# Kernel tuning notes

Measured on AMD Instinct MI355X. Metric: run time of the kernel, lower is better.

## Reference

```python
import jax, jax.numpy as jnp
import numpy as np

B, S, D = 1, 2048, 2048
H, KVH, HD = 32, 8, 64
FFN = 8192
N_EXPERTS, TOP_K = 32, 4
EPS = 1e-5
NEG = -1e9


def setup_inputs() -> dict:
    key = jax.random.key(0)
    ks = jax.random.split(key, 24)
    s = 0.02
    inp = {}
    inp['hidden_states'] = jax.random.normal(ks[0], (B, S, D), jnp.float32)
    # RoPE tables: cos/sin of shape [B, S, HD]
    inv_freq = 1.0 / (10000.0 ** (np.arange(0, HD, 2, dtype=np.float32) / HD))
    t = np.arange(S, dtype=np.float32)
    freqs = np.outer(t, inv_freq)                      # [S, HD/2]
    emb = np.concatenate([freqs, freqs], axis=-1)      # [S, HD]
    inp['cos'] = jnp.asarray(np.cos(emb))[None].repeat(B, axis=0)
    inp['sin'] = jnp.asarray(np.sin(emb))[None].repeat(B, axis=0)
    # additive causal mask [B, 1, S, S]
    causal = jnp.where(jnp.tril(jnp.ones((S, S), bool)), 0.0, NEG).astype(jnp.float32)
    inp['attention_mask'] = jnp.broadcast_to(causal[None, None], (B, 1, S, S))
    # attention params
    inp['wq'] = jax.random.normal(ks[1], (H * HD, D), jnp.float32) * s
    inp['bq'] = jnp.zeros((H * HD,), jnp.float32)
    inp['wk'] = jax.random.normal(ks[2], (KVH * HD, D), jnp.float32) * s
    inp['bk'] = jnp.zeros((KVH * HD,), jnp.float32)
    inp['wv'] = jax.random.normal(ks[3], (KVH * HD, D), jnp.float32) * s
    inp['bv'] = jnp.zeros((KVH * HD,), jnp.float32)
    inp['wo'] = jax.random.normal(ks[4], (D, H * HD), jnp.float32) * s
    inp['bo'] = jnp.zeros((D,), jnp.float32)
    # norms
    inp['ln1_w'] = jnp.ones((D,), jnp.float32)
    inp['ln2_w'] = jnp.ones((D,), jnp.float32)
    # MoE gate + shared expert MLP
    inp['gate_w'] = jax.random.normal(ks[5], (N_EXPERTS, D), jnp.float32) * s
    inp['gate_b'] = jnp.zeros((N_EXPERTS,), jnp.float32)
    inp['w1'] = jax.random.normal(ks[6], (FFN, D), jnp.float32) * s
    inp['b1'] = jnp.zeros((FFN,), jnp.float32)
    inp['w2'] = jax.random.normal(ks[7], (D, FFN), jnp.float32) * s
    inp['b2'] = jnp.zeros((D,), jnp.float32)
    inp['w3'] = jax.random.normal(ks[8], (FFN, D), jnp.float32) * s
    inp['b3'] = jnp.zeros((FFN,), jnp.float32)
    return inp


def _rms_norm(x, w, eps=EPS):
    x32 = x.astype(jnp.float32)
    var = jnp.mean(x32 * x32, axis=-1, keepdims=True)
    return (w * (x32 * jax.lax.rsqrt(var + eps))).astype(x.dtype)


def _rotate_half(x):
    x1, x2 = jnp.split(x, 2, axis=-1)
    return jnp.concatenate([-x2, x1], axis=-1)


def _decoder_layer(hidden_states, cos, sin, attention_mask,
                   wq, bq, wk, bk, wv, bv, wo, bo, ln1_w, ln2_w,
                   gate_w, gate_b, w1, b1, w2, b2, w3, b3):
    residual = hidden_states
    x = _rms_norm(hidden_states, ln1_w)

    # projections -> [B, heads, S, HD]
    q = (x @ wq.T + bq).reshape(B, S, H, HD).transpose(0, 2, 1, 3)
    k = (x @ wk.T + bk).reshape(B, S, KVH, HD).transpose(0, 2, 1, 3)
    v = (x @ wv.T + bv).reshape(B, S, KVH, HD).transpose(0, 2, 1, 3)

    # RoPE (cos/sin unsqueezed on head dim)
    c, s_ = cos[:, None], sin[:, None]
    q = q * c + _rotate_half(q) * s_
    k = k * c + _rotate_half(k) * s_

    # GQA: repeat kv heads
    n_rep = H // KVH
    k = jnp.repeat(k, n_rep, axis=1)
    v = jnp.repeat(v, n_rep, axis=1)

    scaling = HD ** -0.5
    scores = jnp.einsum('bhqd,bhkd->bhqk', q, k) * scaling + attention_mask
    probs = jax.nn.softmax(scores.astype(jnp.float32), axis=-1).astype(q.dtype)
    attn = jnp.einsum('bhqk,bhkd->bhqd', probs, v)
    attn = attn.transpose(0, 2, 1, 3).reshape(B, S, H * HD)
    attn = attn @ wo.T + bo

    hidden_states = residual + attn
    residual = hidden_states
    x = _rms_norm(hidden_states, ln2_w)

    # MoE block (as written in source: router computed, but ALL tokens go
    # through one shared expert MLP; routing weights unused in output)
    flat = x.reshape(-1, D)
    router_logits = flat @ gate_w.T + gate_b                     # [B*S, E]
    rw = jax.nn.softmax(router_logits.astype(jnp.float32), axis=-1)
    rw_top, sel = jax.lax.top_k(rw, TOP_K)                       # computed, unused
    del rw_top, sel

    h1 = flat @ w1.T + b1
    h3 = flat @ w3.T + b3
    mlp = (jax.nn.silu(h1) * h3) @ w2.T + b2
    hidden_states = residual + mlp.reshape(B, S, D)
    return hidden_states


def reference(hidden_states, cos, sin, attention_mask,
              wq, bq, wk, bk, wv, bv, wo, bo, ln1_w, ln2_w,
              gate_w, gate_b, w1, b1, w2, b2, w3, b3):
    return _decoder_layer(hidden_states, cos, sin, attention_mask,
                          wq, bq, wk, bk, wv, bv, wo, bo, ln1_w, ln2_w,
                          gate_w, gate_b, w1, b1, w2, b2, w3, b3)
```

## Files before the change

### kernel.cpp

```cpp
#include <hip/hip_runtime.h>

#define S_LEN 2048
#define DMODEL 2048
#define NH 32
#define NKV 8
#define HD 64
#define FFN_DIM 8192

typedef __attribute__((ext_vector_type(4))) float f32x4;
typedef __attribute__((ext_vector_type(16))) float f32x16;
typedef __attribute__((ext_vector_type(8))) short bf16x8;

#define MFMA(a, b, c) __builtin_amdgcn_mfma_f32_16x16x32_bf16(a, b, c, 0, 0, 0)
#define MFMA32(a, b, c) __builtin_amdgcn_mfma_f32_32x32x16_bf16(a, b, c, 0, 0, 0)

__device__ __forceinline__ ushort f2bf(float f) {
  unsigned u = __float_as_uint(f);
  unsigned r = (u + 0x7fffu + ((u >> 16) & 1u)) >> 16;
  return (ushort)r;
}
__device__ __forceinline__ float bf2f(ushort s) {
  return __uint_as_float(((unsigned)s) << 16);
}
__device__ __forceinline__ unsigned cvtpk(float a, float b) {
  unsigned r;
  asm("v_cvt_pk_bf16_f32 %0, %1, %2" : "=v"(r) : "v"(a), "v"(b));
  return r;
}

__device__ __forceinline__ void gload16(const void* g, void* l) {
  __builtin_amdgcn_global_load_lds(
      (const __attribute__((address_space(1))) void*)g,
      (__attribute__((address_space(3))) void*)l, 16, 0, 0);
}

__global__ __launch_bounds__(256) void cvt_k(const float* __restrict__ in,
                                             ushort* __restrict__ out) {
  int i = blockIdx.x * 256 + threadIdx.x;
  f32x4 a = ((const f32x4*)in)[i * 2];
  f32x4 b = ((const f32x4*)in)[i * 2 + 1];
  bf16x8 r;
#pragma unroll
  for (int j = 0; j < 4; j++) r[j] = (short)f2bf(a[j]);
#pragma unroll
  for (int j = 0; j < 4; j++) r[4 + j] = (short)f2bf(b[j]);
  ((bf16x8*)out)[i] = r;
}

__global__ __launch_bounds__(256) void cvt_qkv_k(const float* __restrict__ wq,
                                                 const float* __restrict__ wk,
                                                 const float* __restrict__ wv,
                                                 ushort* __restrict__ dst) {
  int row = blockIdx.x;
  const float* src;
  if (row < 2048) src = wq + (size_t)row * DMODEL;
  else if (row < 2560) src = wk + (size_t)(row - 2048) * DMODEL;
  else src = wv + (size_t)(row - 2560) * DMODEL;
  int i = threadIdx.x * 8;
  f32x4 a = *(const f32x4*)(src + i);
  f32x4 b = *(const f32x4*)(src + i + 4);
  bf16x8 r;
#pragma unroll
  for (int j = 0; j < 4; j++) r[j] = (short)f2bf(a[j]);
#pragma unroll
  for (int j = 0; j < 4; j++) r[4 + j] = (short)f2bf(b[j]);
  *(bf16x8*)(dst + (size_t)row * DMODEL + i) = r;
}

__global__ __launch_bounds__(256) void bias3_k(const float* __restrict__ a,
                                               const float* __restrict__ b,
                                               const float* __restrict__ c,
                                               float* __restrict__ out) {
  int i = blockIdx.x * 256 + threadIdx.x;
  float v;
  if (i < 2048) v = a[i];
  else if (i < 2560) v = b[i - 2048];
  else v = c[i - 2560];
  out[i] = v;
}

__global__ __launch_bounds__(256) void rmsnorm_k(const float* __restrict__ in,
                                                 const float* __restrict__ w,
                                                 ushort* __restrict__ out) {
  const int row = blockIdx.x;
  const int tid = threadIdx.x;
  const float* x = in + (size_t)row * DMODEL;
  f32x4 v0 = *(const f32x4*)(x + tid * 8);
  f32x4 v1 = *(const f32x4*)(x + tid * 8 + 4);
  float ss = v0[0] * v0[0] + v0[1] * v0[1] + v0[2] * v0[2] + v0[3] * v0[3] +
             v1[0] * v1[0] + v1[1] * v1[1] + v1[2] * v1[2] + v1[3] * v1[3];
#pragma unroll
  for (int off = 32; off; off >>= 1) ss += __shfl_xor(ss, off, 64);
  __shared__ float red[4];
  if ((tid & 63) == 0) red[tid >> 6] = ss;
  __syncthreads();
  float tot = red[0] + red[1] + red[2] + red[3];
  float inv = rsqrtf(tot * (1.f / DMODEL) + 1e-5f);
#pragma unroll
  for (int i = 0; i < 8; i++) {
    int c = tid * 8 + i;
    float val = (i < 4) ? v0[i] : v1[i - 4];
    out[(size_t)row * DMODEL + c] = f2bf(w[c] * val * inv);
  }
}

__global__ __launch_bounds__(256) void rope_k(ushort* __restrict__ qkv,
                                              const float* __restrict__ cs,
                                              const float* __restrict__ sn) {
  int idx = blockIdx.x * 256 + threadIdx.x;
  int d = idx & 31;
  int t = idx >> 5;
  int head = t % (NH + NKV);
  int s = t / (NH + NKV);
  int col = (head < NH) ? head * HD : DMODEL + (head - NH) * HD;
  ushort* p = qkv + (size_t)s * 3072 + col;
  float lo = bf2f(p[d]), hi = bf2f(p[d + 32]);
  float c = cs[s * HD + d], si = sn[s * HD + d];
  p[d] = f2bf(lo * c - hi * si);
  p[d + 32] = f2bf(hi * c + lo * si);
}

enum { EPI_BF16 = 0, EPI_RESID = 1, EPI_SILU = 2, EPI_MUL = 3, EPI_PART = 4 };

__device__ __forceinline__ void quad(const bf16x8* Arr, const bf16x8* BR,
                                     f32x4 (*accr)[4], int qn) {
#pragma unroll
  for (int i = 0; i < 4; i++)
#pragma unroll
    for (int j = 0; j < 2; j++)
#pragma unroll
      for (int ks = 0; ks < 2; ks++)
        accr[i][qn * 2 + j] =
            MFMA(Arr[2 * i + ks], BR[2 * j + ks], accr[i][qn * 2 + j]);
}

template <int EPI>
__global__ __launch_bounds__(512, 2) void gemm256(
    const ushort* __restrict__ A, int lda, const ushort* __restrict__ B,
    int ldb, const float* __restrict__ bias, const float* __restrict__ resid,
    ushort* __restrict__ outb, float* __restrict__ outf, int ldc, int K,
    int kspan, long long opart) {
  __shared__ __align__(16) ushort lds[65536];
  const int tid = threadIdx.x;
  const int l = tid & 63, w = tid >> 6;
  const int g = l >> 4, r16 = l & 15;
  const int wm = w >> 2, wn = w & 3;

  int nwg = gridDim.x * gridDim.y;
  int bid = blockIdx.y * gridDim.x + blockIdx.x;
  bid = (bid & 7) * (nwg >> 3) + (bid >> 3);
  const int m0 = (bid % gridDim.x) * 256;
  const int n0 = (bid / gridDim.x) * 256;
  const int z = blockIdx.z;

  const ushort* Ag = A + (size_t)z * kspan + (size_t)m0 * lda;
  const ushort* Bg = B + (size_t)z * kspan + (size_t)n0 * ldb;
  ushort* outbz = outb;
  if (EPI == EPI_PART) outbz = outb + (size_t)z * opart;

  const int NT = K >> 6;

  const int stgRow = w * 8 + (l >> 3);
  const int stgCol = ((l & 7) ^ (l >> 3)) * 8;

  const int xa = (r16 & 7) << 4;
  const int c0 = ((g * 16) ^ xa) >> 1;
  const int c1 = c0 ^ 32;
  const int slotA = wm ? 3 : 1;
  const int slotB = (wn >> 1) ? 2 : 0;
  const ushort* pA0 = lds + slotA * 8192 + r16 * 64 + c0;
  const ushort* pA1 = lds + slotA * 8192 + r16 * 64 + c1;
  const ushort* pB0 = lds + slotB * 8192 + ((wn & 1) * 64 + r16) * 64 + c0;
  const ushort* pB1 = lds + slotB * 8192 + ((wn & 1) * 64 + r16) * 64 + c1;

  f32x4 acc[8][4];
#pragma unroll
  for (int i = 0; i < 8; i++)
#pragma unroll
    for (int j = 0; j < 4; j++) acc[i][j] = (f32x4){0, 0, 0, 0};

  auto stageA = [&](int slot, int tile, int hf) {
    ushort* dst = lds + ((tile & 1) * 32768 + slot * 8192 + w * 512);
    const ushort* src =
        Ag + (size_t)(hf * 128 + stgRow) * lda + tile * 64 + stgCol;
    gload16(src, dst);
    gload16(src + (size_t)64 * lda, dst + 4096);
  };
  auto stageB = [&](int slot, int tile, int hf) {
    ushort* dst = lds + ((tile & 1) * 32768 + slot * 8192 + w * 512);
    const ushort* src =
        Bg + (size_t)(hf * 128 + stgRow) * ldb + tile * 64 + stgCol;
    gload16(src, dst);
    gload16(src + (size_t)64 * ldb, dst + 4096);
  };

  stageB(0, 0, 0);
  stageA(1, 0, 0);
  stageB(2, 0, 1);
  stageA(3, 0, 1);
  stageB(0, 1, 0);
  stageA(1, 1, 0);
  asm volatile("s_waitcnt vmcnt(4)" ::: "memory");
  __builtin_amdgcn_s_barrier();

  bf16x8 Ar[8], Br0[4], Br1[4];

  for (int t = 0; t < NT; ++t) {
    const int bo = (t & 1) * 32768;
#pragma unroll
    for (int i = 0; i < 4; i++) {
      Ar[2 * i] = *(const bf16x8*)(pA0 + bo + i * 1024);
      Ar[2 * i + 1] = *(const bf16x8*)(pA1 + bo + i * 1024);
    }
#pragma unroll
    for (int j = 0; j < 2; j++) {
      Br0[2 * j] = *(const bf16x8*)(pB0 + bo + j * 1024);
      Br0[2 * j + 1] = *(const bf16x8*)(pB1 + bo + j * 1024);
    }
    if (t + 1 < NT) stageB(2, t + 1, 1);
    __builtin_amdgcn_s_barrier();
    __builtin_amdgcn_s_setprio(1);
    quad(Ar, Br0, &acc[0], 0);
    __builtin_amdgcn_s_setprio(0);
    __builtin_amdgcn_s_barrier();
#pragma unroll
    for (int j = 0; j < 2; j++) {
      Br1[2 * j] = *(const bf16x8*)(pB0 + bo + (j + 2) * 1024);
      Br1[2 * j + 1] = *(const bf16x8*)(pB1 + bo + (j + 2) * 1024);
    }
    if (t + 1 < NT) stageA(3, t + 1, 1);
    __builtin_amdgcn_s_barrier();
    __builtin_amdgcn_s_setprio(1);
    quad(Ar, Br1, &acc[0], 1);
    __builtin_amdgcn_s_setprio(0);
    __builtin_amdgcn_s_barrier();
#pragma unroll
    for (int i = 0; i < 4; i++) {
      Ar[2 * i] = *(const bf16x8*)(pA0 + bo + (i + 4) * 1024);
      Ar[2 * i + 1] = *(const bf16x8*)(pA1 + bo + (i + 4) * 1024);
    }
    if (t + 2 < NT) stageB(0, t + 2, 0);
    __builtin_amdgcn_s_barrier();
    __builtin_amdgcn_s_setprio(1);
    quad(Ar, Br1, &acc[4], 1);
    __builtin_amdgcn_s_setprio(0);
    __builtin_amdgcn_s_barrier();
    if (t + 2 < NT) stageA(1, t + 2, 0);
    __builtin_amdgcn_s_barrier();
    __builtin_amdgcn_s_setprio(1);
    quad(Ar, Br0, &acc[4], 0);
    __builtin_amdgcn_s_setprio(0);
    if (t + 2 < NT) {
      asm volatile("s_waitcnt vmcnt(4)" ::: "memory");
    } else {
      asm volatile("s_waitcnt vmcnt(0)" ::: "memory");
    }
    __builtin_amdgcn_s_barrier();
  }

#pragma unroll
  for (int mf = 0; mf < 8; mf++) {
#pragma unroll
    for (int nf = 0; nf < 4; nf++) {
      const int n = n0 + wn * 64 + nf * 16 + r16;
      float bia = (EPI == EPI_PART) ? 0.f : bias[n];
#pragma unroll
      for (int reg = 0; reg < 4; reg++) {
        const int m = m0 + wm * 128 + mf * 16 + g * 4 + reg;
        float v = acc[mf][nf][reg] + bia;
        if constexpr (EPI == EPI_BF16) {
          outbz[(size_t)m * ldc + n] = f2bf(v);
        } else if constexpr (EPI == EPI_RESID) {
          outf[(size_t)m * ldc + n] = v + resid[(size_t)m * ldc + n];
        } else if constexpr (EPI == EPI_SILU) {
          float sv = v / (1.f + __expf(-v));
          outbz[(size_t)m * ldc + n] = f2bf(sv);
        } else if constexpr (EPI == EPI_MUL) {
          float hv = bf2f(outbz[(size_t)m * ldc + n]);
          outbz[(size_t)m * ldc + n] = f2bf(v * hv);
        } else {
          outbz[(size_t)m * ldc + n] = f2bf(v);
        }
      }
    }
  }
}

template <int MODE>
__global__ __launch_bounds__(256) void reduce2_k(
    const ushort* __restrict__ part, long long pstride, int nz,
    const float* __restrict__ bias, int ncol, const float* __restrict__ resid,
    float* __restrict__ outf, ushort* __restrict__ outb) {
  long long i = (long long)(blockIdx.x * 256 + threadIdx.x) * 8;
  int col = (int)(i % ncol);
  float s[8];
#pragma unroll
  for (int j = 0; j < 8; j++) s[j] = bias[col + j];
  for (int zz = 0; zz < nz; zz++) {
    bf16x8 v = *(const bf16x8*)(part + zz * pstride + i);
#pragma unroll
    for (int j = 0; j < 8; j++) s[j] += bf2f((ushort)v[j]);
  }
  if constexpr (MODE == 1) {
#pragma unroll
    for (int j = 0; j < 8; j++) outf[i + j] = s[j] + resid[i + j];
  } else {
    bf16x8 r;
#pragma unroll
    for (int j = 0; j < 8; j++) r[j] = (short)f2bf(s[j]);
    *(bf16x8*)(outb + i) = r;
  }
}

__global__ __launch_bounds__(256, 3) void flash2_k(const ushort* __restrict__ qkv,
                                                   ushort* __restrict__ att) {
  const int bid = blockIdx.x;
  const int head = (bid >> 4) & 31;
  const int rmap = bid & 15;
  const int qb = (bid & 256) ? (15 - rmap) : rmap;
  const int kvh = head >> 2;
  const int tid = threadIdx.x;
  const int w = tid >> 6, l = tid & 63;
  const int h = l >> 5, q31 = l & 31;
  const int qw = qb * 128 + w * 32;
  const int qrow = qw + q31;

  __shared__ __align__(16) ushort lds[2][8192];

  bf16x8 qreg[4];
  {
    const ushort* qp = qkv + (size_t)qrow * 3072 + head * HD;
#pragma unroll
    for (int s = 0; s < 4; s++)
      qreg[s] = *(const bf16x8*)(qp + s * 16 + h * 8);
  }

  f32x16 oacc[2];
#pragma unroll
  for (int i = 0; i < 16; i++) { oacc[0][i] = 0.f; oacc[1][i] = 0.f; }
  float mreg = -1e30f, lsum = 0.f;

  const int nt = 2 * qb + 2;

  const int skv = tid >> 2;
  const int sch = (tid & 3) * 2;
  const int vkv = tid & 63;
  const int vd0 = (tid >> 6) * 16;

  const ushort* kg_base = qkv + DMODEL + kvh * HD;

  bf16x8 krA, krB, vrA, vrB;
  auto loadTile = [&](int jb) {
    const ushort* kg = kg_base + (size_t)jb * 64 * 3072;
    krA = *(const bf16x8*)(kg + (size_t)skv * 3072 + sch * 8);
    krB = *(const bf16x8*)(kg + (size_t)skv * 3072 + sch * 8 + 8);
    const ushort* vg = kg + 512;
    vrA = *(const bf16x8*)(vg + (size_t)vkv * 3072 + vd0);
    vrB = *(const bf16x8*)(vg + (size_t)vkv * 3072 + vd0 + 8);
  };
  auto writeTile = [&](int b) {
    ushort* kb = lds[b];
    *(bf16x8*)(kb + skv * 64 + ((sch ^ (skv & 7)) * 8)) = krA;
    *(bf16x8*)(kb + skv * 64 + (((sch + 1) ^ (skv & 7)) * 8)) = krB;
    ushort* vb = lds[b] + 4096;
#pragma unroll
    for (int i = 0; i < 8; i++) {
      int d = vd0 + i;
      vb[d * 64 + (((vkv >> 3) ^ (d & 7)) * 8) + (vkv & 7)] = (ushort)vrA[i];
    }
#pragma unroll
    for (int i = 0; i < 8; i++) {
      int d = vd0 + 8 + i;
      vb[d * 64 + (((vkv >> 3) ^ (d & 7)) * 8) + (vkv & 7)] = (ushort)vrB[i];
    }
  };

  loadTile(0);
  for (int jb = 0; jb < nt; ++jb) {
    const int b = jb & 1;
    writeTile(b);
    __syncthreads();
    if (jb + 1 < nt) loadTile(jb + 1);

    if (jb * 64 <= qw + 31) {
      const ushort* Kb = lds[b];
      const ushort* Vb = lds[b] + 4096;

      f32x16 sacc[2];
#pragma unroll
      for (int i = 0; i < 16; i++) { sacc[0][i] = 0.f; sacc[1][i] = 0.f; }
#pragma unroll
      for (int c = 0; c < 2; c++) {
        const int kvr = c * 32 + q31;
        const ushort* kp = Kb + kvr * 64;
        const int kx = kvr & 7;
#pragma unroll
        for (int s = 0; s < 4; s++) {
          bf16x8 kf = *(const bf16x8*)(kp + ((2 * s + h) ^ kx) * 8);
          sacc[c] = MFMA32(kf, qreg[s], sacc[c]);
        }
      }

      const bool diag = (jb * 64 + 63 > qw);
      if (diag) {
#pragma unroll
        for (int c = 0; c < 2; c++)
#pragma unroll
          for (int rg = 0; rg < 16; rg++) {
            int kvg = jb * 64 + c * 32 + (rg & 3) + 8 * (rg >> 2) + 4 * h;
            if (kvg > qrow) sacc[c][rg] = -1e30f;
          }
      }
      float tmax = sacc[0][0];
#pragma unroll
      for (int rg = 1; rg < 16; rg++) tmax = fmaxf(tmax, sacc[0][rg]);
#pragma unroll
      for (int rg = 0; rg < 16; rg++) tmax = fmaxf(tmax, sacc[1][rg]);
      tmax = fmaxf(tmax, __shfl_xor(tmax, 32));
      const float mn = fmaxf(mreg, tmax);
      const float resc = __expf((mreg - mn) * 0.125f);
      mreg = mn;
      float rsum = 0.f;
#pragma unroll
      for (int c = 0; c < 2; c++)
#pragma unroll
        for (int rg = 0; rg < 16; rg++) {
          float pv = __expf((sacc[c][rg] - mn) * 0.125f);
          sacc[c][rg] = pv;
          rsum += pv;
        }
      rsum += __shfl_xor(rsum, 32);
      lsum = lsum * resc + rsum;
      oacc[0] *= resc;
      oacc[1] *= resc;

      unsigned pw_[2][4][2];
#pragma unroll
      for (int c = 0; c < 2; c++)
#pragma unroll
        for (int rr = 0; rr < 4; rr++) {
          pw_[c][rr][0] = cvtpk(sacc[c][4 * rr + 0], sacc[c][4 * rr + 1]);
          pw_[c][rr][1] = cvtpk(sacc[c][4 * rr + 2], sacc[c][4 * rr + 3]);
        }

#pragma unroll
      for (int s = 0; s < 4; s++) {
        const int c = s >> 1, base = (s & 1) * 2;
        unsigned k0 = h ? pw_[c][base + 1][0] : pw_[c][base][0];
        unsigned k1 = h ? pw_[c][base + 1][1] : pw_[c][base][1];
        unsigned s0 = h ? pw_[c][base][0] : pw_[c][base + 1][0];
        unsigned s1 = h ? pw_[c][base][1] : pw_[c][base + 1][1];
        unsigned t0 = __shfl_xor(s0, 32);
        unsigned t1 = __shfl_xor(s1, 32);
        union { unsigned u[4]; bf16x8 v; } pf;
        pf.u[0] = h ? t0 : k0;
        pf.u[1] = h ? t1 : k1;
        pf.u[2] = h ? k0 : t0;
        pf.u[3] = h ? k1 : t1;
#pragma unroll
        for (int dt = 0; dt < 2; dt++) {
          const int d = dt * 32 + q31;
          bf16x8 vf =
              *(const bf16x8*)(Vb + d * 64 + ((2 * s + h) ^ (d & 7)) * 8);
          oacc[dt] = MFMA32(vf, pf.v, oacc[dt]);
        }
      }
    }
  }

  const float inv = 1.f / lsum;
  ushort* op = att + (size_t)qrow * DMODEL + head * HD;
#pragma unroll
  for (int dt = 0; dt < 2; dt++)
#pragma unroll
    for (int rr = 0; rr < 4; rr++) {
      const int d0 = dt * 32 + 8 * rr + 4 * h;
      unsigned lo = cvtpk(oacc[dt][4 * rr + 0] * inv, oacc[dt][4 * rr + 1] * inv);
      unsigned hi = cvtpk(oacc[dt][4 * rr + 2] * inv, oacc[dt][4 * rr + 3] * inv);
      uint2 v2;
      v2.x = lo;
      v2.y = hi;
      *(uint2*)(op + d0) = v2;
    }
}

extern "C" void kernel_launch(void* const* d_in, const int* in_sizes, int n_in,
                              void* d_out, int out_size, void* d_ws,
                              size_t ws_size, hipStream_t stream) {
  (void)in_sizes; (void)n_in; (void)out_size; (void)ws_size;
  const float* hidden = (const float*)d_in[0];
  const float* cosb = (const float*)d_in[1];
  const float* sinb = (const float*)d_in[2];
  const float* wq = (const float*)d_in[4];
  const float* bq = (const float*)d_in[5];
  const float* wk = (const float*)d_in[6];
  const float* bk = (const float*)d_in[7];
  const float* wv = (const float*)d_in[8];
  const float* bv = (const float*)d_in[9];
  const float* wo = (const float*)d_in[10];
  const float* bo = (const float*)d_in[11];
  const float* ln1 = (const float*)d_in[12];
  const float* ln2 = (const float*)d_in[13];
  const float* w1 = (const float*)d_in[16];
  const float* b1 = (const float*)d_in[17];
  const float* w2 = (const float*)d_in[18];
  const float* b2 = (const float*)d_in[19];
  const float* w3 = (const float*)d_in[20];
  const float* b3 = (const float*)d_in[21];
  float* out = (float*)d_out;

  char* ws = (char*)d_ws;
  ushort* x1 = (ushort*)ws;   ws += (size_t)S_LEN * DMODEL * 2;
  ushort* qkv = (ushort*)ws;  ws += (size_t)S_LEN * 3072 * 2;
  ushort* att = (ushort*)ws;  ws += (size_t)S_LEN * DMODEL * 2;
  ushort* x2 = (ushort*)ws;   ws += (size_t)S_LEN * DMODEL * 2;
  ushort* hbuf = (ushort*)ws; ws += (size_t)S_LEN * FFN_DIM * 2;
  ushort* wbuf = (ushort*)ws; ws += (size_t)FFN_DIM * DMODEL * 2;
  float* bqkv = (float*)ws;   ws += 3072 * 4;

  ushort* partQ = att;
  ushort* partO = x2;
  ushort* partW = x1;

  rmsnorm_k<<<S_LEN, 256, 0, stream>>>(hidden, ln1, x1);

  cvt_qkv_k<<<3072, 256, 0, stream>>>(wq, wk, wv, wbuf);
  bias3_k<<<12, 256, 0, stream>>>(bq, bk, bv, bqkv);

  gemm256<EPI_PART><<<dim3(8, 12, 2), 512, 0, stream>>>(
      x1, DMODEL, wbuf, DMODEL, nullptr, nullptr, partQ, nullptr, 3072, 1024,
      1024, (long long)S_LEN * 3072);
  reduce2_k<0><<<(S_LEN * 3072) / 2048, 256, 0, stream>>>(
      partQ, (long long)S_LEN * 3072, 2, bqkv, 3072, nullptr, nullptr, qkv);

  rope_k<<<(S_LEN * (NH + NKV) * 32) / 256, 256, 0, stream>>>(qkv, cosb, sinb);

  flash2_k<<<512, 256, 0, stream>>>(qkv, att);

  cvt_k<<<(2048 * 2048) / 2048, 256, 0, stream>>>(wo, wbuf);
  gemm256<EPI_PART><<<dim3(8, 8, 4), 512, 0, stream>>>(
      att, DMODEL, wbuf, DMODEL, nullptr, nullptr, partO, nullptr, DMODEL, 512,
      512, (long long)S_LEN * DMODEL);
  reduce2_k<1><<<(S_LEN * DMODEL) / 2048, 256, 0, stream>>>(
      partO, (long long)S_LEN * DMODEL, 4, bo, DMODEL, hidden, out, nullptr);

  rmsnorm_k<<<S_LEN, 256, 0, stream>>>(out, ln2, x2);

  cvt_k<<<(FFN_DIM * 2048) / 2048, 256, 0, stream>>>(w1, wbuf);
  gemm256<EPI_SILU><<<dim3(8, 32), 512, 0, stream>>>(
      x2, DMODEL, wbuf, DMODEL, b1, nullptr, hbuf, nullptr, FFN_DIM, DMODEL, 0,
      0);

  cvt_k<<<(FFN_DIM * 2048) / 2048, 256, 0, stream>>>(w3, wbuf);
  gemm256<EPI_MUL><<<dim3(8, 32), 512, 0, stream>>>(
      x2, DMODEL, wbuf, DMODEL, b3, nullptr, hbuf, nullptr, FFN_DIM, DMODEL, 0,
      0);

  cvt_k<<<(DMODEL * FFN_DIM) / 2048, 256, 0, stream>>>(w2, wbuf);
  gemm256<EPI_PART><<<dim3(8, 8, 4), 512, 0, stream>>>(
      hbuf, FFN_DIM, wbuf, FFN_DIM, nullptr, nullptr, partW, nullptr, DMODEL,
      DMODEL, DMODEL, (long long)S_LEN * DMODEL);
  reduce2_k<1><<<(S_LEN * DMODEL) / 2048, 256, 0, stream>>>(
      partW, (long long)S_LEN * DMODEL, 4, b2, DMODEL, out, out, nullptr);
}
```

Baseline: 425.3 us.

## Prefetch full tiles two iterations ahead and fence LDS reads per MFMA cluster

Changes the GEMM software pipeline so that both halves of the A and B tiles are prefetched two K-iterations ahead, instead of splitting the second halves one iteration ahead. The vmcnt wait goes from 4 to 8 outstanding loads to match. It also wraps each MFMA cluster in a helper that waits for LDS reads and adds a scheduling barrier, so register loads finish before the math starts. The aim is to hide global-load latency behind more work, at the cost of more loads in flight and more rigid instruction scheduling.

```diff
diff --git a/kernel.cpp b/kernel.cpp
--- a/kernel.cpp
+++ b/kernel.cpp
@@ -134,6 +134,17 @@
             MFMA(Arr[2 * i + ks], BR[2 * j + ks], accr[i][qn * 2 + j]);
 }
 
+__device__ __forceinline__ void cluster_begin() {
+  __builtin_amdgcn_s_barrier();
+  asm volatile("s_waitcnt lgkmcnt(0)" ::: "memory");
+  __builtin_amdgcn_sched_barrier(0);
+  __builtin_amdgcn_s_setprio(1);
+}
+__device__ __forceinline__ void cluster_end() {
+  __builtin_amdgcn_s_setprio(0);
+  __builtin_amdgcn_s_barrier();
+}
+
 template <int EPI>
 __global__ __launch_bounds__(512, 2) void gemm256(
     const ushort* __restrict__ A, int lda, const ushort* __restrict__ B,
@@ -195,12 +206,14 @@
   };
 
   stageB(0, 0, 0);
+  stageB(2, 0, 1);
   stageA(1, 0, 0);
-  stageB(2, 0, 1);
   stageA(3, 0, 1);
   stageB(0, 1, 0);
+  stageB(2, 1, 1);
   stageA(1, 1, 0);
-  asm volatile("s_waitcnt vmcnt(4)" ::: "memory");
+  stageA(3, 1, 1);
+  asm volatile("s_waitcnt vmcnt(8)" ::: "memory");
   __builtin_amdgcn_s_barrier();
 
   bf16x8 Ar[8], Br0[4], Br1[4];
@@ -217,41 +230,39 @@
       Br0[2 * j] = *(const bf16x8*)(pB0 + bo + j * 1024);
       Br0[2 * j + 1] = *(const bf16x8*)(pB1 + bo + j * 1024);
     }
-    if (t + 1 < NT) stageB(2, t + 1, 1);
-    __builtin_amdgcn_s_barrier();
-    __builtin_amdgcn_s_setprio(1);
+    cluster_begin();
     quad(Ar, Br0, &acc[0], 0);
-    __builtin_amdgcn_s_setprio(0);
-    __builtin_amdgcn_s_barrier();
+    cluster_end();
 #pragma unroll
     for (int j = 0; j < 2; j++) {
       Br1[2 * j] = *(const bf16x8*)(pB0 + bo + (j + 2) * 1024);
       Br1[2 * j + 1] = *(const bf16x8*)(pB1 + bo + (j + 2) * 1024);
     }
-    if (t + 1 < NT) stageA(3, t + 1, 1);
-    __builtin_amdgcn_s_barrier();
-    __builtin_amdgcn_s_setprio(1);
+    cluster_begin();
     quad(Ar, Br1, &acc[0], 1);
-    __builtin_amdgcn_s_setprio(0);
-    __builtin_amdgcn_s_barrier();
+    cluster_end();
 #pragma unroll
     for (int i = 0; i < 4; i++) {
       Ar[2 * i] = *(const bf16x8*)(pA0 + bo + (i + 4) * 1024);
       Ar[2 * i + 1] = *(const bf16x8*)(pA1 + bo + (i + 4) * 1024);
     }
-    if (t + 2 < NT) stageB(0, t + 2, 0);
-    __builtin_amdgcn_s_barrier();
-    __builtin_amdgcn_s_setprio(1);
+    if (t + 2 < NT) {
+      stageB(0, t + 2, 0);
+      stageB(2, t + 2, 1);
+    }
+    cluster_begin();
     quad(Ar, Br1, &acc[4], 1);
-    __builtin_amdgcn_s_setprio(0);
-    __builtin_amdgcn_s_barrier();
-    if (t + 2 < NT) stageA(1, t + 2, 0);
+    cluster_end();
+    if (t + 2 < NT) {
+      stageA(1, t + 2, 0);
+      stageA(3, t + 2, 1);
+    }
     __builtin_amdgcn_s_barrier();
     __builtin_amdgcn_s_setprio(1);
     quad(Ar, Br0, &acc[4], 0);
     __builtin_amdgcn_s_setprio(0);
     if (t + 2 < NT) {
-      asm volatile("s_waitcnt vmcnt(4)" ::: "memory");
+      asm volatile("s_waitcnt vmcnt(8)" ::: "memory");
     } else {
       asm volatile("s_waitcnt vmcnt(0)" ::: "memory");
     }
```

Result: no change. 430.0 us (+1.1%).

## Restructure GEMM main loop into software-pipelined two-tile phases with register prefetch

Applied to the files above, without the earlier changes.

Rewrites the 256x256 bf16 GEMM main loop to process two K-tiles per iteration, using separate register sets for even and odd A fragments and prefetching LDS fragments for the next phase while the current MFMA quad runs. Global staging now prefetches both halves of a tile ahead, with full vmcnt drains at tile boundaries, and scheduling barriers plus lgkmcnt waits pin the instruction order. The aim is to hide LDS read latency and global-load latency behind MFMA work. The cost is higher register pressure and a fixed lgkmcnt count that must match the number of LDS reads actually issued. The loop also assumes an even tile count.

```diff
diff --git a/kernel.cpp b/kernel.cpp
--- a/kernel.cpp
+++ b/kernel.cpp
@@ -122,17 +122,31 @@
 
 enum { EPI_BF16 = 0, EPI_RESID = 1, EPI_SILU = 2, EPI_MUL = 3, EPI_PART = 4 };
 
-__device__ __forceinline__ void quad(const bf16x8* Arr, const bf16x8* BR,
-                                     f32x4 (*accr)[4], int qn) {
-#pragma unroll
-  for (int i = 0; i < 4; i++)
-#pragma unroll
-    for (int j = 0; j < 2; j++)
-#pragma unroll
-      for (int ks = 0; ks < 2; ks++)
-        accr[i][qn * 2 + j] =
-            MFMA(Arr[2 * i + ks], BR[2 * j + ks], accr[i][qn * 2 + j]);
-}
+#define QUAD(AS, BS, MROW, NCOL)                                     \
+  _Pragma("unroll") for (int mf_ = 0; mf_ < 4; mf_++)                \
+  _Pragma("unroll") for (int nf_ = 0; nf_ < 2; nf_++)                \
+  _Pragma("unroll") for (int kk_ = 0; kk_ < 2; kk_++)                \
+      acc[(MROW) + mf_][(NCOL) + nf_] =                              \
+          MFMA(AS[2 * mf_ + kk_], BS[2 * nf_ + kk_],                 \
+               acc[(MROW) + mf_][(NCOL) + nf_]);
+
+#define PHASE_SYNC                                   \
+  __builtin_amdgcn_sched_barrier(0);                 \
+  __builtin_amdgcn_s_barrier();                      \
+  asm volatile("s_waitcnt lgkmcnt(6)" ::: "memory"); \
+  __builtin_amdgcn_sched_barrier(0);                 \
+  __builtin_amdgcn_s_setprio(1);
+
+#define PHASE_END                                    \
+  __builtin_amdgcn_s_setprio(0);                     \
+  __builtin_amdgcn_sched_barrier(0);                 \
+  __builtin_amdgcn_s_barrier();
+
+#define PHASE_END_DRAIN                              \
+  __builtin_amdgcn_s_setprio(0);                     \
+  __builtin_amdgcn_sched_barrier(0);                 \
+  asm volatile("s_waitcnt vmcnt(0)" ::: "memory");   \
+  __builtin_amdgcn_s_barrier();
 
 template <int EPI>
 __global__ __launch_bounds__(512, 2) void gemm256(
@@ -158,7 +172,7 @@
   ushort* outbz = outb;
   if (EPI == EPI_PART) outbz = outb + (size_t)z * opart;
 
-  const int NT = K >> 6;
+  const int NT = K >> 6, NI = NT >> 1;
 
   const int stgRow = w * 8 + (l >> 3);
   const int stgCol = ((l & 7) ^ (l >> 3)) * 8;
@@ -166,12 +180,16 @@
   const int xa = (r16 & 7) << 4;
   const int c0 = ((g * 16) ^ xa) >> 1;
   const int c1 = c0 ^ 32;
-  const int slotA = wm ? 3 : 1;
-  const int slotB = (wn >> 1) ? 2 : 0;
-  const ushort* pA0 = lds + slotA * 8192 + r16 * 64 + c0;
-  const ushort* pA1 = lds + slotA * 8192 + r16 * 64 + c1;
-  const ushort* pB0 = lds + slotB * 8192 + ((wn & 1) * 64 + r16) * 64 + c0;
-  const ushort* pB1 = lds + slotB * 8192 + ((wn & 1) * 64 + r16) * 64 + c1;
+  const int aslot = wm ? 24576 : 8192;
+  const int bslot = ((wn >> 1) ? 16384 : 0) + (wn & 1) * 4096;
+  const ushort* pA0b0 = lds + aslot + r16 * 64 + c0;
+  const ushort* pA1b0 = lds + aslot + r16 * 64 + c1;
+  const ushort* pA0b1 = pA0b0 + 32768;
+  const ushort* pA1b1 = pA1b0 + 32768;
+  const ushort* pB0b0 = lds + bslot + r16 * 64 + c0;
+  const ushort* pB1b0 = lds + bslot + r16 * 64 + c1;
+  const ushort* pB0b1 = pB0b0 + 32768;
+  const ushort* pB1b1 = pB1b0 + 32768;
 
   f32x4 acc[8][4];
 #pragma unroll
@@ -200,62 +218,98 @@
   stageA(3, 0, 1);
   stageB(0, 1, 0);
   stageA(1, 1, 0);
-  asm volatile("s_waitcnt vmcnt(4)" ::: "memory");
+  stageB(2, 1, 1);
+  stageA(3, 1, 1);
+  asm volatile("s_waitcnt vmcnt(8)" ::: "memory");
   __builtin_amdgcn_s_barrier();
 
-  bf16x8 Ar[8], Br0[4], Br1[4];
-
-  for (int t = 0; t < NT; ++t) {
-    const int bo = (t & 1) * 32768;
-#pragma unroll
-    for (int i = 0; i < 4; i++) {
-      Ar[2 * i] = *(const bf16x8*)(pA0 + bo + i * 1024);
-      Ar[2 * i + 1] = *(const bf16x8*)(pA1 + bo + i * 1024);
-    }
-#pragma unroll
-    for (int j = 0; j < 2; j++) {
-      Br0[2 * j] = *(const bf16x8*)(pB0 + bo + j * 1024);
-      Br0[2 * j + 1] = *(const bf16x8*)(pB1 + bo + j * 1024);
-    }
-    if (t + 1 < NT) stageB(2, t + 1, 1);
-    __builtin_amdgcn_s_barrier();
-    __builtin_amdgcn_s_setprio(1);
-    quad(Ar, Br0, &acc[0], 0);
-    __builtin_amdgcn_s_setprio(0);
-    __builtin_amdgcn_s_barrier();
-#pragma unroll
-    for (int j = 0; j < 2; j++) {
-      Br1[2 * j] = *(const bf16x8*)(pB0 + bo + (j + 2) * 1024);
-      Br1[2 * j + 1] = *(const bf16x8*)(pB1 + bo + (j + 2) * 1024);
-    }
-    if (t + 1 < NT) stageA(3, t + 1, 1);
-    __builtin_amdgcn_s_barrier();
-    __builtin_amdgcn_s_setprio(1);
-    quad(Ar, Br1, &acc[0], 1);
-    __builtin_amdgcn_s_setprio(0);
-    __builtin_amdgcn_s_barrier();
-#pragma unroll
-    for (int i = 0; i < 4; i++) {
-      Ar[2 * i] = *(const bf16x8*)(pA0 + bo + (i + 4) * 1024);
-      Ar[2 * i + 1] = *(const bf16x8*)(pA1 + bo + (i + 4) * 1024);
-    }
-    if (t + 2 < NT) stageB(0, t + 2, 0);
-    __builtin_amdgcn_s_barrier();
-    __builtin_amdgcn_s_setprio(1);
-    quad(Ar, Br1, &acc[4], 1);
-    __builtin_amdgcn_s_setprio(0);
-    __builtin_amdgcn_s_barrier();
-    if (t + 2 < NT) stageA(1, t + 2, 0);
-    __builtin_amdgcn_s_barrier();
-    __builtin_amdgcn_s_setprio(1);
-    quad(Ar, Br0, &acc[4], 0);
-    __builtin_amdgcn_s_setprio(0);
-    if (t + 2 < NT) {
-      asm volatile("s_waitcnt vmcnt(4)" ::: "memory");
-    } else {
-      asm volatile("s_waitcnt vmcnt(0)" ::: "memory");
-    }
-    __builtin_amdgcn_s_barrier();
+  bf16x8 Ae[8], Ao[8], Bp0[4], Bp1[4], Bq[4];
+#pragma unroll
+  for (int j = 0; j < 4; j++) {
+    Ae[2 * j] = *(const bf16x8*)(pA0b0 + j * 1024);
+    Ae[2 * j + 1] = *(const bf16x8*)(pA1b0 + j * 1024);
+  }
+#pragma unroll
+  for (int nf = 0; nf < 2; nf++) {
+    Bp0[2 * nf] = *(const bf16x8*)(pB0b0 + nf * 1024);
+    Bp0[2 * nf + 1] = *(const bf16x8*)(pB1b0 + nf * 1024);
+  }
+
+  for (int i = 0; i < NI; ++i) {
+    const bool st = (i + 1 < NI);
+    const int t2 = 2 * i + 2, t3 = 2 * i + 3;
+    Bq[0] = *(const bf16x8*)(pB0b0 + 2 * 1024);
+    Bq[1] = *(const bf16x8*)(pB1b0 + 2 * 1024);
+    Bq[2] = *(const bf16x8*)(pB0b0 + 3 * 1024);
+    Bq[3] = *(const bf16x8*)(pB1b0 + 3 * 1024);
+    Ao[0] = *(const bf16x8*)(pA0b0 + 4 * 1024);
+    Ao[1] = *(const bf16x8*)(pA1b0 + 4 * 1024);
+    PHASE_SYNC; QUAD(Ae, Bp0, 0, 0); PHASE_END;
+    Ao[2] = *(const bf16x8*)(pA0b0 + 5 * 1024);
+    Ao[3] = *(const bf16x8*)(pA1b0 + 5 * 1024);
+    Ao[4] = *(const bf16x8*)(pA0b0 + 6 * 1024);
+    Ao[5] = *(const bf16x8*)(pA1b0 + 6 * 1024);
+    Ao[6] = *(const bf16x8*)(pA0b0 + 7 * 1024);
+    Ao[7] = *(const bf16x8*)(pA1b0 + 7 * 1024);
+    PHASE_SYNC; QUAD(Ae, Bq, 0, 2); PHASE_END_DRAIN;
+    Ae[0] = *(const bf16x8*)(pA0b1 + 0 * 1024);
+    Ae[1] = *(const bf16x8*)(pA1b1 + 0 * 1024);
+    Ae[2] = *(const bf16x8*)(pA0b1 + 1 * 1024);
+    Ae[3] = *(const bf16x8*)(pA1b1 + 1 * 1024);
+    Ae[4] = *(const bf16x8*)(pA0b1 + 2 * 1024);
+    Ae[5] = *(const bf16x8*)(pA1b1 + 2 * 1024);
+    if (st) {
+      stageB(0, t2, 0);
+      stageB(2, t2, 1);
+    }
+    PHASE_SYNC; QUAD(Ao, Bq, 4, 2); PHASE_END;
+    Ae[6] = *(const bf16x8*)(pA0b1 + 3 * 1024);
+    Ae[7] = *(const bf16x8*)(pA1b1 + 3 * 1024);
+    Bp1[0] = *(const bf16x8*)(pB0b1 + 0 * 1024);
+    Bp1[1] = *(const bf16x8*)(pB1b1 + 0 * 1024);
+    Bp1[2] = *(const bf16x8*)(pB0b1 + 1 * 1024);
+    Bp1[3] = *(const bf16x8*)(pB1b1 + 1 * 1024);
+    if (st) {
+      stageA(1, t2, 0);
+      stageA(3, t2, 1);
+    }
+    PHASE_SYNC; QUAD(Ao, Bp0, 4, 0); PHASE_END;
+    Bq[0] = *(const bf16x8*)(pB0b1 + 2 * 1024);
+    Bq[1] = *(const bf16x8*)(pB1b1 + 2 * 1024);
+    Bq[2] = *(const bf16x8*)(pB0b1 + 3 * 1024);
+    Bq[3] = *(const bf16x8*)(pB1b1 + 3 * 1024);
+    Ao[0] = *(const bf16x8*)(pA0b1 + 4 * 1024);
+    Ao[1] = *(const bf16x8*)(pA1b1 + 4 * 1024);
+    PHASE_SYNC; QUAD(Ae, Bp1, 0, 0); PHASE_END;
+    Ao[2] = *(const bf16x8*)(pA0b1 + 5 * 1024);
+    Ao[3] = *(const bf16x8*)(pA1b1 + 5 * 1024);
+    Ao[4] = *(const bf16x8*)(pA0b1 + 6 * 1024);
+    Ao[5] = *(const bf16x8*)(pA1b1 + 6 * 1024);
+    Ao[6] = *(const bf16x8*)(pA0b1 + 7 * 1024);
+    Ao[7] = *(const bf16x8*)(pA1b1 + 7 * 1024);
+    PHASE_SYNC; QUAD(Ae, Bq, 0, 2); PHASE_END_DRAIN;
+    Ae[0] = *(const bf16x8*)(pA0b0 + 0 * 1024);
+    Ae[1] = *(const bf16x8*)(pA1b0 + 0 * 1024);
+    Ae[2] = *(const bf16x8*)(pA0b0 + 1 * 1024);
+    Ae[3] = *(const bf16x8*)(pA1b0 + 1 * 1024);
+    Ae[4] = *(const bf16x8*)(pA0b0 + 2 * 1024);
+    Ae[5] = *(const bf16x8*)(pA1b0 + 2 * 1024);
+    if (st) {
+      stageB(0, t3, 0);
+      stageB(2, t3, 1);
+    }
+    PHASE_SYNC; QUAD(Ao, Bq, 4, 2); PHASE_END;
+    Ae[6] = *(const bf16x8*)(pA0b0 + 3 * 1024);
+    Ae[7] = *(const bf16x8*)(pA1b0 + 3 * 1024);
+    Bp0[0] = *(const bf16x8*)(pB0b0 + 0 * 1024);
+    Bp0[1] = *(const bf16x8*)(pB1b0 + 0 * 1024);
+    Bp0[2] = *(const bf16x8*)(pB0b0 + 1 * 1024);
+    Bp0[3] = *(const bf16x8*)(pB1b0 + 1 * 1024);
+    if (st) {
+      stageA(1, t3, 0);
+      stageA(3, t3, 1);
+    }
+    PHASE_SYNC; QUAD(Ao, Bp1, 4, 0); PHASE_END;
   }
 
 #pragma unroll
```

After: 428.9 us. Within noise of the previous version (+0.9%).

## Unroll GEMM main loop by two with explicit phase scheduling barriers

Applied to the files above, without the earlier changes.

Restructures the 256x256 bf16 GEMM main loop to process two K-tiles per iteration, using fixed LDS buffer pointers instead of computing a buffer offset each iteration. It reorders global-to-LDS staging so that B halves are issued before A halves, and wraps each MFMA phase in sched_barrier, s_barrier and lgkmcnt waits to pin the instruction order. The aim is to cut address arithmetic and let the compiler interleave loads with MFMAs less freely, improving overlap. It assumes NT is even, and the added waits could serialize work if the vmcnt accounting does not match the new staging order.

```diff
diff --git a/kernel.cpp b/kernel.cpp
--- a/kernel.cpp
+++ b/kernel.cpp
@@ -122,17 +122,36 @@
 
 enum { EPI_BF16 = 0, EPI_RESID = 1, EPI_SILU = 2, EPI_MUL = 3, EPI_PART = 4 };
 
-__device__ __forceinline__ void quad(const bf16x8* Arr, const bf16x8* BR,
-                                     f32x4 (*accr)[4], int qn) {
-#pragma unroll
-  for (int i = 0; i < 4; i++)
-#pragma unroll
-    for (int j = 0; j < 2; j++)
-#pragma unroll
-      for (int ks = 0; ks < 2; ks++)
-        accr[i][qn * 2 + j] =
-            MFMA(Arr[2 * i + ks], BR[2 * j + ks], accr[i][qn * 2 + j]);
-}
+#define QUAD(AS, BS, MROW, NCOL)                                     \
+  _Pragma("unroll") for (int kk_ = 0; kk_ < 2; kk_++)                \
+  _Pragma("unroll") for (int mf_ = 0; mf_ < 4; mf_++)                \
+  _Pragma("unroll") for (int nf_ = 0; nf_ < 2; nf_++)                \
+      acc[(MROW) + mf_][(NCOL) + nf_] =                              \
+          MFMA(AS[2 * mf_ + kk_], BS[2 * nf_ + kk_],                 \
+               acc[(MROW) + mf_][(NCOL) + nf_]);
+
+#define PHASE_MID                                    \
+  __builtin_amdgcn_sched_barrier(0);                 \
+  __builtin_amdgcn_s_barrier();                      \
+  asm volatile("s_waitcnt lgkmcnt(0)" ::: "memory"); \
+  __builtin_amdgcn_sched_barrier(0);                 \
+  __builtin_amdgcn_s_setprio(1);
+
+#define PHASE_CLOSE                                  \
+  __builtin_amdgcn_s_setprio(0);                     \
+  __builtin_amdgcn_sched_barrier(0);                 \
+  __builtin_amdgcn_s_barrier();
+
+#define RD_A(PA0, PA1, J0)                                        \
+  _Pragma("unroll") for (int j_ = 0; j_ < 4; j_++) {              \
+    A_[2 * j_] = *(const bf16x8*)((PA0) + ((J0) + j_) * 1024);    \
+    A_[2 * j_ + 1] = *(const bf16x8*)((PA1) + ((J0) + j_) * 1024);\
+  }
+#define RD_B(DST, PB0, PB1, J0)                                   \
+  _Pragma("unroll") for (int n_ = 0; n_ < 2; n_++) {              \
+    DST[2 * n_] = *(const bf16x8*)((PB0) + ((J0) + n_) * 1024);   \
+    DST[2 * n_ + 1] = *(const bf16x8*)((PB1) + ((J0) + n_) * 1024);\
+  }
 
 template <int EPI>
 __global__ __launch_bounds__(512, 2) void gemm256(
@@ -158,7 +177,7 @@
   ushort* outbz = outb;
   if (EPI == EPI_PART) outbz = outb + (size_t)z * opart;
 
-  const int NT = K >> 6;
+  const int NT = K >> 6, NI = NT >> 1;
 
   const int stgRow = w * 8 + (l >> 3);
   const int stgCol = ((l & 7) ^ (l >> 3)) * 8;
@@ -166,12 +185,16 @@
   const int xa = (r16 & 7) << 4;
   const int c0 = ((g * 16) ^ xa) >> 1;
   const int c1 = c0 ^ 32;
-  const int slotA = wm ? 3 : 1;
-  const int slotB = (wn >> 1) ? 2 : 0;
-  const ushort* pA0 = lds + slotA * 8192 + r16 * 64 + c0;
-  const ushort* pA1 = lds + slotA * 8192 + r16 * 64 + c1;
-  const ushort* pB0 = lds + slotB * 8192 + ((wn & 1) * 64 + r16) * 64 + c0;
-  const ushort* pB1 = lds + slotB * 8192 + ((wn & 1) * 64 + r16) * 64 + c1;
+  const int aslot = wm ? 24576 : 8192;
+  const int bslot = ((wn >> 1) ? 16384 : 0) + (wn & 1) * 4096;
+  const ushort* pA0b0 = lds + aslot + r16 * 64 + c0;
+  const ushort* pA1b0 = lds + aslot + r16 * 64 + c1;
+  const ushort* pA0b1 = pA0b0 + 32768;
+  const ushort* pA1b1 = pA1b0 + 32768;
+  const ushort* pB0b0 = lds + bslot + r16 * 64 + c0;
+  const ushort* pB1b0 = lds + bslot + r16 * 64 + c1;
+  const ushort* pB0b1 = pB0b0 + 32768;
+  const ushort* pB1b1 = pB1b0 + 32768;
 
   f32x4 acc[8][4];
 #pragma unroll
@@ -195,66 +218,56 @@
   };
 
   stageB(0, 0, 0);
+  stageB(2, 0, 1);
   stageA(1, 0, 0);
-  stageB(2, 0, 1);
   stageA(3, 0, 1);
   stageB(0, 1, 0);
-  stageA(1, 1, 0);
+  stageB(2, 1, 1);
   asm volatile("s_waitcnt vmcnt(4)" ::: "memory");
   __builtin_amdgcn_s_barrier();
 
-  bf16x8 Ar[8], Br0[4], Br1[4];
-
-  for (int t = 0; t < NT; ++t) {
-    const int bo = (t & 1) * 32768;
-#pragma unroll
-    for (int i = 0; i < 4; i++) {
-      Ar[2 * i] = *(const bf16x8*)(pA0 + bo + i * 1024);
-      Ar[2 * i + 1] = *(const bf16x8*)(pA1 + bo + i * 1024);
-    }
-#pragma unroll
-    for (int j = 0; j < 2; j++) {
-      Br0[2 * j] = *(const bf16x8*)(pB0 + bo + j * 1024);
-      Br0[2 * j + 1] = *(const bf16x8*)(pB1 + bo + j * 1024);
-    }
-    if (t + 1 < NT) stageB(2, t + 1, 1);
-    __builtin_amdgcn_s_barrier();
-    __builtin_amdgcn_s_setprio(1);
-    quad(Ar, Br0, &acc[0], 0);
+  bf16x8 A_[8], Blo[4], Bhi[4];
+
+  for (int i = 0; i < NI; ++i) {
+    const int ta = 2 * i, tb = 2 * i + 1;
+    const bool st = (ta + 2 < NT);
+    RD_A(pA0b0, pA1b0, 0);
+    RD_B(Blo, pB0b0, pB1b0, 0);
+    stageA(1, tb, 0);
+    asm volatile("s_waitcnt lgkmcnt(8)" ::: "memory");
+    PHASE_MID; QUAD(A_, Blo, 0, 0); PHASE_CLOSE;
+    RD_B(Bhi, pB0b0, pB1b0, 2);
+    stageA(3, tb, 1);
+    PHASE_MID; QUAD(A_, Bhi, 0, 2); PHASE_CLOSE;
+    RD_A(pA0b0, pA1b0, 4);
+    if (st) stageB(0, ta + 2, 0);
+    PHASE_MID; QUAD(A_, Bhi, 4, 2); PHASE_CLOSE;
+    if (st) stageB(2, ta + 2, 1);
+    PHASE_MID; QUAD(A_, Blo, 4, 0);
     __builtin_amdgcn_s_setprio(0);
-    __builtin_amdgcn_s_barrier();
-#pragma unroll
-    for (int j = 0; j < 2; j++) {
-      Br1[2 * j] = *(const bf16x8*)(pB0 + bo + (j + 2) * 1024);
-      Br1[2 * j + 1] = *(const bf16x8*)(pB1 + bo + (j + 2) * 1024);
-    }
-    if (t + 1 < NT) stageA(3, t + 1, 1);
-    __builtin_amdgcn_s_barrier();
-    __builtin_amdgcn_s_setprio(1);
-    quad(Ar, Br1, &acc[0], 1);
-    __builtin_amdgcn_s_setprio(0);
-    __builtin_amdgcn_s_barrier();
-#pragma unroll
-    for (int i = 0; i < 4; i++) {
-      Ar[2 * i] = *(const bf16x8*)(pA0 + bo + (i + 4) * 1024);
-      Ar[2 * i + 1] = *(const bf16x8*)(pA1 + bo + (i + 4) * 1024);
-    }
-    if (t + 2 < NT) stageB(0, t + 2, 0);
-    __builtin_amdgcn_s_barrier();
-    __builtin_amdgcn_s_setprio(1);
-    quad(Ar, Br1, &acc[4], 1);
-    __builtin_amdgcn_s_setprio(0);
-    __builtin_amdgcn_s_barrier();
-    if (t + 2 < NT) stageA(1, t + 2, 0);
-    __builtin_amdgcn_s_barrier();
-    __builtin_amdgcn_s_setprio(1);
-    quad(Ar, Br0, &acc[4], 0);
-    __builtin_amdgcn_s_setprio(0);
-    if (t + 2 < NT) {
+    __builtin_amdgcn_sched_barrier(0);
+    if (st) {
       asm volatile("s_waitcnt vmcnt(4)" ::: "memory");
     } else {
       asm volatile("s_waitcnt vmcnt(0)" ::: "memory");
     }
+    __builtin_amdgcn_s_barrier();
+    RD_A(pA0b1, pA1b1, 0);
+    RD_B(Blo, pB0b1, pB1b1, 0);
+    if (st) stageA(1, ta + 2, 0);
+    asm volatile("s_waitcnt lgkmcnt(8)" ::: "memory");
+    PHASE_MID; QUAD(A_, Blo, 0, 0); PHASE_CLOSE;
+    RD_B(Bhi, pB0b1, pB1b1, 2);
+    if (st) stageA(3, ta + 2, 1);
+    PHASE_MID; QUAD(A_, Bhi, 0, 2); PHASE_CLOSE;
+    RD_A(pA0b1, pA1b1, 4);
+    if (st) stageB(0, tb + 2, 0);
+    PHASE_MID; QUAD(A_, Bhi, 4, 2); PHASE_CLOSE;
+    if (st) stageB(2, tb + 2, 1);
+    PHASE_MID; QUAD(A_, Blo, 4, 0);
+    __builtin_amdgcn_s_setprio(0);
+    __builtin_amdgcn_sched_barrier(0);
+    asm volatile("s_waitcnt vmcnt(4)" ::: "memory");
     __builtin_amdgcn_s_barrier();
   }
 
```

Result: no change. 424.4 us (-0.2%).
